# Performance work log

Measured on AMD Instinct MI355X. Metric: run time of the kernel, lower is better.

The kernel has to match this reference:

```python
import jax, jax.numpy as jnp
import numpy as np

N_HEAD, D_MODEL, D_HEAD = 16, 1024, 64
SCALE = 1.0 / (D_HEAD ** 0.5)
LN_EPS = 1e-5


def _rel_shift(x):
    # x: [b, n, i, j] -> Transformer-XL relative shift
    b, n, i, j = x.shape
    zero_pad = jnp.zeros((b, n, i, 1), x.dtype)
    x_padded = jnp.concatenate([zero_pad, x], axis=3).reshape(b, n, j + 1, i)
    return x_padded[:, :, 1:, :].reshape(b, n, i, j)


def setup_inputs() -> dict:
    key = jax.random.key(0)
    ks = jax.random.split(key, 16)
    qlen, bsz, mem_len = 1024, 2, 1024
    klen = qlen + mem_len
    rlen = klen
    s = 0.02
    inp = {
        'w': jax.random.normal(ks[0], (qlen, bsz, D_MODEL), jnp.float32),
        'r': jax.random.normal(ks[1], (rlen, D_MODEL), jnp.float32),
        'mems': jax.random.normal(ks[2], (mem_len, bsz, D_MODEL), jnp.float32),
        'r_w_bias': s * jax.random.normal(ks[3], (N_HEAD, D_HEAD), jnp.float32),
        'r_r_bias': s * jax.random.normal(ks[4], (N_HEAD, D_HEAD), jnp.float32),
        # causal mask with memory offset: position i attends to j <= i + mem_len
        'attn_mask': jnp.triu(jnp.ones((qlen, klen), bool), k=1 + mem_len),
        'Wq': s * jax.random.normal(ks[5], (D_MODEL, N_HEAD * D_HEAD), jnp.float32),
        'bq': jnp.zeros((N_HEAD * D_HEAD,), jnp.float32),
        'Wk': s * jax.random.normal(ks[6], (D_MODEL, N_HEAD * D_HEAD), jnp.float32),
        'bk': jnp.zeros((N_HEAD * D_HEAD,), jnp.float32),
        'Wv': s * jax.random.normal(ks[7], (D_MODEL, N_HEAD * D_HEAD), jnp.float32),
        'bv': jnp.zeros((N_HEAD * D_HEAD,), jnp.float32),
        'Wr': s * jax.random.normal(ks[8], (D_MODEL, N_HEAD * D_HEAD), jnp.float32),
        'br': jnp.zeros((N_HEAD * D_HEAD,), jnp.float32),
        'Wo': s * jax.random.normal(ks[9], (N_HEAD * D_HEAD, D_MODEL), jnp.float32),
        'bo': jnp.zeros((D_MODEL,), jnp.float32),
        'ln_g': jnp.ones((D_MODEL,), jnp.float32),
        'ln_b': jnp.zeros((D_MODEL,), jnp.float32),
    }
    return inp


def reference(w, r, mems, r_w_bias, r_r_bias, Wq, bq, Wk, bk, Wv, bv, Wr, br, Wo, bo, ln_g, ln_b, attn_mask):
    qlen, bsz, _ = w.shape
    cat = jnp.concatenate([mems, w], axis=0)                      # [klen, b, d_model]
    klen = cat.shape[0]
    q = (cat @ Wq + bq)[-qlen:].reshape(qlen, bsz, N_HEAD, D_HEAD)
    k = (cat @ Wk + bk).reshape(klen, bsz, N_HEAD, D_HEAD)
    v = (cat @ Wv + bv).reshape(klen, bsz, N_HEAD, D_HEAD)
    rk = (r @ Wr + br).reshape(-1, N_HEAD, D_HEAD)               # [rlen, n, d]

    AC = jnp.einsum('ibnd,jbnd->bnij', q + r_w_bias, k)          # content term
    BD = _rel_shift(jnp.einsum('ibnd,jnd->bnij', q + r_r_bias, rk))  # relative term
    attn_score = SCALE * (AC + BD)                                # [b, n, i, j]
    attn_score = jnp.where(attn_mask[None, None, :, :], -jnp.inf, attn_score)
    attn_prob = jax.nn.softmax(attn_score, axis=3)
    attn_vec = jnp.einsum('bnij,jbnd->ibnd', attn_prob, v).reshape(qlen, bsz, N_HEAD * D_HEAD)
    attn_out = attn_vec @ Wo + bo

    res = w + attn_out                                            # post-LN (pre_lnorm=False)
    mu = jnp.mean(res, axis=-1, keepdims=True)
    var = jnp.var(res, axis=-1, keepdims=True)
    return (res - mu) / jnp.sqrt(var + LN_EPS) * ln_g + ln_b
```

## Files before the change

### kernel.cpp

```cpp
#include <hip/hip_runtime.h>
#include <math.h>

#define N_HEADC 16
#define D_MODELC 1024
#define D_HEADC 64
#define QLENC 1024
#define BSZC 2
#define MEMLENC 1024
#define KLENC 2048
#define SCALEC 0.125f
#define SL2C 0.18033688011112042f
#define LN_EPSC 1e-5f
#define RINGC 192

typedef __attribute__((ext_vector_type(8))) short short8;
typedef __attribute__((ext_vector_type(4))) float f32x4;

#define MFMA16(a, b, c) __builtin_amdgcn_mfma_f32_16x16x32_bf16((a), (b), (c), 0, 0, 0)

__device__ inline unsigned short f2bf(float x) {
    union { float f; unsigned int u; } c; c.f = x;
    unsigned int r = c.u + 0x7FFFu + ((c.u >> 16) & 1u);
    return (unsigned short)(r >> 16);
}
__device__ inline float bf2f(short s) {
    union { unsigned int u; float f; } c; c.u = ((unsigned int)(unsigned short)s) << 16;
    return c.f;
}

__device__ __forceinline__ void load_lds16(const short* g, short* l) {
    __builtin_amdgcn_global_load_lds(
        (const __attribute__((address_space(1))) void*)g,
        (__attribute__((address_space(3))) void*)l,
        16, 0, 0);
}

__global__ __launch_bounds__(256) void cast_cat_kernel(
    const float* __restrict__ s0, const float* __restrict__ s1, int splitElems,
    short* __restrict__ dst)
{
    int idx = (blockIdx.x * 256 + threadIdx.x) * 8;
    const float* src = (idx < splitElems) ? (s0 + idx) : (s1 + (idx - splitElems));
    short8 o;
    #pragma unroll
    for (int e = 0; e < 8; ++e) o[e] = (short)f2bf(src[e]);
    *(short8*)(dst + idx) = o;
}

__global__ __launch_bounds__(256) void tcast5_kernel(
    const float* __restrict__ W0, const float* __restrict__ W1,
    const float* __restrict__ W2, const float* __restrict__ W3,
    const float* __restrict__ W4,
    short* __restrict__ D0, short* __restrict__ D1, short* __restrict__ D2,
    short* __restrict__ D3, short* __restrict__ D4)
{
    __shared__ short tile[64][72];
    const float* W; short* D;
    switch (blockIdx.z) {
        case 0: W = W0; D = D0; break;
        case 1: W = W1; D = D1; break;
        case 2: W = W2; D = D2; break;
        case 3: W = W3; D = D3; break;
        default: W = W4; D = D4; break;
    }
    const int t = threadIdx.x;
    const int n0 = blockIdx.x * 64, k0 = blockIdx.y * 64;
    #pragma unroll
    for (int it = 0; it < 2; ++it) {
        int idx = t + it * 256;
        int kl = idx >> 3, c8 = idx & 7;
        const float* src = W + (size_t)(k0 + kl) * D_MODELC + n0 + c8 * 8;
        short8 s;
        #pragma unroll
        for (int e = 0; e < 8; ++e) s[e] = (short)f2bf(src[e]);
        *(short8*)&tile[kl][c8 * 8] = s;
    }
    __syncthreads();
    #pragma unroll
    for (int it = 0; it < 2; ++it) {
        int idx = t + it * 256;
        int nl = idx >> 3, c8 = idx & 7;
        short8 s;
        #pragma unroll
        for (int e = 0; e < 8; ++e) s[e] = tile[c8 * 8 + e][nl];
        *(short8*)(D + (size_t)(n0 + nl) * D_MODELC + k0 + c8 * 8) = s;
    }
}

__global__ __launch_bounds__(256) void vtrans_kernel(
    const short* __restrict__ v_bf, short* __restrict__ vt)
{
    __shared__ short tile[64][72];
    const int t = threadIdx.x;
    const int j0 = blockIdx.x * 64;
    const int bn = blockIdx.y;
    const int b = bn & 1, n = bn >> 1;
    #pragma unroll
    for (int it = 0; it < 2; ++it) {
        int idx = t + it * 256;
        int jl = idx >> 3, c8 = idx & 7;
        short8 s = *(const short8*)(v_bf + ((size_t)(j0 + jl) * 2 + b) * D_MODELC + n * 64 + c8 * 8);
        *(short8*)&tile[jl][c8 * 8] = s;
    }
    __syncthreads();
    #pragma unroll
    for (int it = 0; it < 2; ++it) {
        int idx = t + it * 256;
        int dl = idx >> 3, c8 = idx & 7;
        short8 s;
        #pragma unroll
        for (int e = 0; e < 8; ++e) s[e] = tile[c8 * 8 + e][dl];
        *(short8*)(vt + ((size_t)(b * 16 + n) * 64 + dl) * (size_t)KLENC + j0 + c8 * 8) = s;
    }
}

__global__ __launch_bounds__(256, 3) void proj_gemm_kernel(
    const short* __restrict__ cat, const short* __restrict__ rin,
    const short* __restrict__ WqT, const short* __restrict__ WkT,
    const short* __restrict__ WvT, const short* __restrict__ WrT,
    const float* __restrict__ bq, const float* __restrict__ bk,
    const float* __restrict__ bv, const float* __restrict__ br,
    const float* __restrict__ rwb, const float* __restrict__ rrb,
    short* __restrict__ qw, short* __restrict__ qr,
    short* __restrict__ kb, short* __restrict__ vb, short* __restrict__ rk)
{
    __shared__ short As[128][32];
    __shared__ short Bs[128][32];

    const int lin = blockIdx.y * 8 + blockIdx.x;
    const int sw  = (lin & 7) * 96 + (lin >> 3);
    const int bx  = sw & 7;
    const int by  = sw >> 3;

    const short* A; const short* Bt; const float* bias; int yt, mode;
    if (by < 32)      { A = cat;                         Bt = WkT; bias = bk; yt = by;      mode = 0; }
    else if (by < 64) { A = cat;                         Bt = WvT; bias = bv; yt = by - 32; mode = 1; }
    else if (by < 80) { A = cat + (size_t)2048 * 1024;   Bt = WqT; bias = bq; yt = by - 64; mode = 2; }
    else              { A = rin;                         Bt = WrT; bias = br; yt = by - 80; mode = 3; }

    const int row0 = yt * 128, col0 = bx * 128;
    const int t = threadIdx.x;
    const int lane = t & 63, wid = t >> 6;
    const int row16 = lane & 15, g8 = lane >> 4;
    const int wr = wid >> 1, wc = wid & 1;

    f32x4 acc[4][4];
    #pragma unroll
    for (int m = 0; m < 4; ++m)
        #pragma unroll
        for (int nn = 0; nn < 4; ++nn)
            acc[m][nn] = (f32x4){0.f, 0.f, 0.f, 0.f};

    short* AsB = &As[0][0] + wid * 1024;
    short* BsB = &Bs[0][0] + wid * 1024;
    const int srow4 = lane >> 2;
    const int cs4 = (lane & 3) ^ ((lane >> 3) & 3);
    const short* Ag = A  + (size_t)(row0 + wid * 32 + srow4) * D_MODELC + cs4 * 8;
    const short* Bg = Bt + (size_t)(col0 + wid * 32 + srow4) * D_MODELC + cs4 * 8;
    const int xc2 = (row16 >> 1) & 3;

    for (int k0 = 0; k0 < D_MODELC; k0 += 32) {
        load_lds16(Ag + k0,              AsB);
        load_lds16(Ag + k0 + 16 * 1024,  AsB + 512);
        load_lds16(Bg + k0,              BsB);
        load_lds16(Bg + k0 + 16 * 1024,  BsB + 512);
        __syncthreads();
        short8 af[4], bfr[4];
        #pragma unroll
        for (int m = 0; m < 4; ++m)
            af[m] = *(const short8*)&As[wr * 64 + m * 16 + row16][(g8 ^ xc2) * 8];
        #pragma unroll
        for (int nn = 0; nn < 4; ++nn)
            bfr[nn] = *(const short8*)&Bs[wc * 64 + nn * 16 + row16][(g8 ^ xc2) * 8];
        #pragma unroll
        for (int m = 0; m < 4; ++m)
            #pragma unroll
            for (int nn = 0; nn < 4; ++nn)
                acc[m][nn] = MFMA16(af[m], bfr[nn], acc[m][nn]);
        __syncthreads();
    }

    float bvv[4], w1[4], w2[4];
    #pragma unroll
    for (int nn = 0; nn < 4; ++nn) {
        int c = col0 + wc * 64 + nn * 16 + row16;
        bvv[nn] = bias[c];
        w1[nn] = rwb[c];
        w2[nn] = rrb[c];
    }
    if (mode == 2) {
        #pragma unroll
        for (int m = 0; m < 4; ++m)
            #pragma unroll
            for (int nn = 0; nn < 4; ++nn) {
                int c = col0 + wc * 64 + nn * 16 + row16;
                #pragma unroll
                for (int reg = 0; reg < 4; ++reg) {
                    int r = row0 + wr * 64 + m * 16 + g8 * 4 + reg;
                    float v = acc[m][nn][reg] + bvv[nn];
                    qw[(size_t)r * D_MODELC + c] = (short)f2bf(v + w1[nn]);
                    qr[(size_t)r * D_MODELC + c] = (short)f2bf(v + w2[nn]);
                }
            }
    } else {
        short* C = (mode == 0) ? kb : (mode == 1) ? vb : rk;
        #pragma unroll
        for (int m = 0; m < 4; ++m)
            #pragma unroll
            for (int nn = 0; nn < 4; ++nn) {
                int c = col0 + wc * 64 + nn * 16 + row16;
                #pragma unroll
                for (int reg = 0; reg < 4; ++reg) {
                    int r = row0 + wr * 64 + m * 16 + g8 * 4 + reg;
                    C[(size_t)r * D_MODELC + c] = (short)f2bf(acc[m][nn][reg] + bvv[nn]);
                }
            }
    }
}

__global__ __launch_bounds__(256, 3) void wo_gemm_kernel(
    const short* __restrict__ A, const short* __restrict__ Bt,
    float* __restrict__ out0, float* __restrict__ out1)
{
    __shared__ short As[128][32];
    __shared__ short Bs[128][32];
    const int kz = blockIdx.z;
    float* C = kz ? out1 : out0;
    const int row0 = blockIdx.y * 128, col0 = blockIdx.x * 128;
    const int t = threadIdx.x;
    const int lane = t & 63, wid = t >> 6;
    const int row16 = lane & 15, g8 = lane >> 4;
    const int wr = wid >> 1, wc = wid & 1;

    f32x4 acc[4][4];
    #pragma unroll
    for (int m = 0; m < 4; ++m)
        #pragma unroll
        for (int nn = 0; nn < 4; ++nn)
            acc[m][nn] = (f32x4){0.f, 0.f, 0.f, 0.f};

    short* AsB = &As[0][0] + wid * 1024;
    short* BsB = &Bs[0][0] + wid * 1024;
    const int srow4 = lane >> 2;
    const int cs4 = (lane & 3) ^ ((lane >> 3) & 3);
    const short* Ag = A  + (size_t)(row0 + wid * 32 + srow4) * D_MODELC + cs4 * 8;
    const short* Bg = Bt + (size_t)(col0 + wid * 32 + srow4) * D_MODELC + cs4 * 8;
    const int xc2 = (row16 >> 1) & 3;

    const int kbase = kz * 512;
    for (int k0 = kbase; k0 < kbase + 512; k0 += 32) {
        load_lds16(Ag + k0,             AsB);
        load_lds16(Ag + k0 + 16 * 1024, AsB + 512);
        load_lds16(Bg + k0,             BsB);
        load_lds16(Bg + k0 + 16 * 1024, BsB + 512);
        __syncthreads();
        short8 af[4], bfr[4];
        #pragma unroll
        for (int m = 0; m < 4; ++m)
            af[m] = *(const short8*)&As[wr * 64 + m * 16 + row16][(g8 ^ xc2) * 8];
        #pragma unroll
        for (int nn = 0; nn < 4; ++nn)
            bfr[nn] = *(const short8*)&Bs[wc * 64 + nn * 16 + row16][(g8 ^ xc2) * 8];
        #pragma unroll
        for (int m = 0; m < 4; ++m)
            #pragma unroll
            for (int nn = 0; nn < 4; ++nn)
                acc[m][nn] = MFMA16(af[m], bfr[nn], acc[m][nn]);
        __syncthreads();
    }

    #pragma unroll
    for (int m = 0; m < 4; ++m)
        #pragma unroll
        for (int nn = 0; nn < 4; ++nn) {
            int c = col0 + wc * 64 + nn * 16 + row16;
            #pragma unroll
            for (int reg = 0; reg < 4; ++reg) {
                int r = row0 + wr * 64 + m * 16 + g8 * 4 + reg;
                C[(size_t)r * D_MODELC + c] = acc[m][nn][reg];
            }
        }
}

__global__ __launch_bounds__(256, 2) void attn_mfma_kernel(
    const short* __restrict__ qw, const short* __restrict__ qr,
    const short* __restrict__ kb, const short* __restrict__ rkb,
    const short* __restrict__ vt, short* __restrict__ av)
{
    __shared__ short Kl[2][64][64];
    __shared__ short Vl[64][64];
    __shared__ short Rl[RINGC][64];
    __shared__ short pun[4][1600];
    __shared__ float scb[4][16];

    const int wave = threadIdx.x >> 6, lane = threadIdx.x & 63;
    const int row16 = lane & 15, g8 = lane >> 4;
    const int srow = lane >> 3, chk = lane & 7;
    const int swz = srow & 7;

    const int lin = blockIdx.y * 16 + blockIdx.x;
    const int xcd = lin & 7;
    const int u   = lin >> 3;
    const int v   = u & 31;
    const int bn  = xcd * 4 + (v >> 3);
    const int tt  = v & 7;
    const int ic  = (u >> 5) ? (15 - tt) : tt;
    const int b = bn & 1, n = bn >> 1;
    const int i0 = ic * 64;
    const int i0w = i0 + wave * 16;

    short8 qwf[2], qrf[2];
    #pragma unroll
    for (int ks = 0; ks < 2; ++ks) {
        size_t off = ((size_t)(i0w + row16) * 2 + b) * D_MODELC + n * 64 + ks * 32 + g8 * 8;
        qwf[ks] = *(const short8*)(qw + off);
        qrf[ks] = *(const short8*)(qr + off);
    }

    #pragma unroll
    for (int t = 0; t < 2; ++t) {
        int rr = wave * 16 + t * 8;
        int j  = rr + srow;
        int cs = chk ^ swz;
        load_lds16(kb + ((size_t)j * 2 + b) * D_MODELC + n * 64 + cs * 8, &Kl[0][rr][0]);
    }
    {
        const int p0 = 960 - i0;
        #pragma unroll
        for (int t = 0; t < 4; ++t) {
            int jrb_ = p0 + wave * 32 + t * 8;
            int slotb = jrb_ % RINGC;
            int jr = jrb_ + srow;
            int jc = jr < KLENC ? jr : KLENC - 1;
            int cs = chk ^ swz;
            load_lds16(rkb + (size_t)jc * D_MODELC + n * 64 + cs * 8, &Rl[slotb][0]);
        }
    }

    f32x4 accO[4];
    #pragma unroll
    for (int dt = 0; dt < 4; ++dt) accO[dt] = (f32x4){0.f, 0.f, 0.f, 0.f};
    float m = -INFINITY, lsum = 0.f;

    const int T = (i0 + 63 + MEMLENC + 64) >> 6;
    const int r7 = row16 & 7;

    __syncthreads();

    for (int s = 0; s < T; ++s) {
        const int j0 = s * 64;
        const int cur = s & 1, nxt = cur ^ 1;

        #pragma unroll
        for (int t = 0; t < 2; ++t) {
            int rr = wave * 16 + t * 8;
            int j  = j0 + 64 + rr + srow;
            if (j > KLENC - 1) j = KLENC - 1;
            int cs = chk ^ swz;
            load_lds16(kb + ((size_t)j * 2 + b) * D_MODELC + n * 64 + cs * 8, &Kl[nxt][rr][0]);
        }
        {
            const int nb = j0 + 1088 - i0;
            #pragma unroll
            for (int t = 0; t < 2; ++t) {
                int jrb_ = nb + wave * 16 + t * 8;
                int slotb = jrb_ % RINGC;
                int jr = jrb_ + srow;
                int jc = jr < KLENC ? jr : KLENC - 1;
                int cs = chk ^ swz;
                load_lds16(rkb + (size_t)jc * D_MODELC + n * 64 + cs * 8, &Rl[slotb][0]);
            }
        }
        #pragma unroll
        for (int t = 0; t < 2; ++t) {
            int rr = wave * 16 + t * 8;
            int cs = chk ^ swz;
            load_lds16(vt + ((size_t)((b * 16 + n) * 64 + rr + srow)) * KLENC + j0 + cs * 8,
                       &Vl[rr][0]);
        }

        f32x4 st[4];
        #pragma unroll
        for (int jt = 0; jt < 4; ++jt) {
            st[jt] = (f32x4){0.f, 0.f, 0.f, 0.f};
            const short* kr = &Kl[cur][jt * 16 + row16][0];
            st[jt] = MFMA16(*(const short8*)(kr + ((g8 ^ r7) * 8)),       qwf[0], st[jt]);
            st[jt] = MFMA16(*(const short8*)(kr + (((4 + g8) ^ r7) * 8)), qwf[1], st[jt]);
        }

        const int jrb_w = j0 - i0w + 1008;
        const int sb = jrb_w % RINGC;
        short* bdT = &pun[wave][0];
        #pragma unroll
        for (int rt = 0; rt < 5; ++rt) {
            int rsl = sb + rt * 16 + row16;
            if (rsl >= RINGC) rsl -= RINGC;
            const short* rr = &Rl[rsl][0];
            f32x4 bd = (f32x4){0.f, 0.f, 0.f, 0.f};
            bd = MFMA16(*(const short8*)(rr + ((g8 ^ r7) * 8)),       qrf[0], bd);
            bd = MFMA16(*(const short8*)(rr + (((4 + g8) ^ r7) * 8)), qrf[1], bd);
            #pragma unroll
            for (int e = 0; e < 4; ++e)
                bdT[(rt * 16 + g8 * 4 + e) * 20 + row16] = (short)f2bf(bd[e]);
        }

        float sl[4][4];
        #pragma unroll
        for (int jt = 0; jt < 4; ++jt)
            #pragma unroll
            for (int reg = 0; reg < 4; ++reg) {
                const int jl = jt * 16 + g8 * 4 + reg;
                float vv = st[jt][reg] + bf2f(bdT[(jl + 15 - row16) * 20 + row16]);
                sl[jt][reg] = (j0 + jl > i0w + row16 + MEMLENC) ? -INFINITY : vv * SL2C;
            }

        float mx0 = fmaxf(fmaxf(sl[0][0], sl[0][1]), fmaxf(sl[0][2], sl[0][3]));
        float mx1 = fmaxf(fmaxf(sl[1][0], sl[1][1]), fmaxf(sl[1][2], sl[1][3]));
        float mx2 = fmaxf(fmaxf(sl[2][0], sl[2][1]), fmaxf(sl[2][2], sl[2][3]));
        float mx3 = fmaxf(fmaxf(sl[3][0], sl[3][1]), fmaxf(sl[3][2], sl[3][3]));
        float mx = fmaxf(fmaxf(mx0, mx1), fmaxf(mx2, mx3));
        mx = fmaxf(mx, __shfl_xor(mx, 16, 64));
        mx = fmaxf(mx, __shfl_xor(mx, 32, 64));

        if (__any(mx > m + 8.f)) {
            float mn = fmaxf(m, mx);
            float sc = exp2f(m - mn);
            m = mn;
            lsum *= sc;
            if (lane < 16) scb[wave][lane] = sc;
            float4 s4 = *(const float4*)&scb[wave][g8 * 4];
            #pragma unroll
            for (int dt = 0; dt < 4; ++dt) {
                accO[dt][0] *= s4.x; accO[dt][1] *= s4.y;
                accO[dt][2] *= s4.z; accO[dt][3] *= s4.w;
            }
        }

        float ps = 0.f;
        #pragma unroll
        for (int jt = 0; jt < 4; ++jt)
            #pragma unroll
            for (int reg = 0; reg < 4; ++reg) {
                float p = exp2f(sl[jt][reg] - m);
                sl[jt][reg] = p;
                ps += p;
            }
        ps += __shfl_xor(ps, 16, 64);
        ps += __shfl_xor(ps, 32, 64);
        lsum += ps;
        short* pP = &pun[wave][0];
        #pragma unroll
        for (int jt = 0; jt < 4; ++jt)
            #pragma unroll
            for (int reg = 0; reg < 4; ++reg) {
                const int ch = (jt * 2 + (g8 >> 1)) ^ r7;
                pP[row16 * 64 + ch * 8 + (g8 & 1) * 4 + reg] = (short)f2bf(sl[jt][reg]);
            }

        __syncthreads();

        #pragma unroll
        for (int ks2 = 0; ks2 < 2; ++ks2) {
            short8 pf = *(const short8*)&pP[row16 * 64 + (((ks2 * 4 + g8) ^ r7) * 8)];
            #pragma unroll
            for (int dt = 0; dt < 4; ++dt) {
                const short* vp = &Vl[dt * 16 + row16][(((ks2 * 4 + g8) ^ r7) * 8)];
                accO[dt] = MFMA16(pf, *(const short8*)vp, accO[dt]);
            }
        }

        __syncthreads();
    }

    if (lane < 16) scb[wave][lane] = lsum;
    float4 l4 = *(const float4*)&scb[wave][g8 * 4];
    float rl4[4] = {1.f / l4.x, 1.f / l4.y, 1.f / l4.z, 1.f / l4.w};
    #pragma unroll
    for (int dt = 0; dt < 4; ++dt)
        #pragma unroll
        for (int reg = 0; reg < 4; ++reg) {
            size_t o = ((size_t)(i0w + g8 * 4 + reg) * 2 + b) * D_MODELC + n * 64 + dt * 16 + row16;
            av[o] = (short)f2bf(accO[dt][reg] * rl4[reg]);
        }
}

__global__ __launch_bounds__(256) void ln_kernel(
    const float* __restrict__ w, const float* __restrict__ ao0,
    const float* __restrict__ ao1, const float* __restrict__ bo,
    const float* __restrict__ g, const float* __restrict__ bb,
    float* __restrict__ out)
{
    __shared__ float red[2][4];
    const int row = blockIdx.x;
    const int lane = threadIdx.x & 63;
    const int wv = threadIdx.x >> 6;
    const size_t base = (size_t)row * D_MODELC;
    const int c = threadIdx.x * 4;

    float4 xw = *(const float4*)&w[base + c];
    float4 x0 = *(const float4*)&ao0[base + c];
    float4 x1 = *(const float4*)&ao1[base + c];
    float4 xb = *(const float4*)&bo[c];
    float x[4] = {xw.x + x0.x + x1.x + xb.x, xw.y + x0.y + x1.y + xb.y,
                  xw.z + x0.z + x1.z + xb.z, xw.w + x0.w + x1.w + xb.w};

    float sum = x[0] + x[1] + x[2] + x[3];
    float ssq = x[0]*x[0] + x[1]*x[1] + x[2]*x[2] + x[3]*x[3];
    #pragma unroll
    for (int off = 32; off > 0; off >>= 1) {
        sum += __shfl_xor(sum, off, 64);
        ssq += __shfl_xor(ssq, off, 64);
    }
    if (lane == 0) { red[0][wv] = sum; red[1][wv] = ssq; }
    __syncthreads();
    sum = red[0][0] + red[0][1] + red[0][2] + red[0][3];
    ssq = red[1][0] + red[1][1] + red[1][2] + red[1][3];

    const float mu = sum * (1.0f / D_MODELC);
    const float var = ssq * (1.0f / D_MODELC) - mu * mu;
    const float rstd = rsqrtf(var + LN_EPSC);

    float4 o;
    o.x = (x[0] - mu) * rstd * g[c] + bb[c];
    o.y = (x[1] - mu) * rstd * g[c+1] + bb[c+1];
    o.z = (x[2] - mu) * rstd * g[c+2] + bb[c+2];
    o.w = (x[3] - mu) * rstd * g[c+3] + bb[c+3];
    *(float4*)&out[base + c] = o;
}

extern "C" void kernel_launch(void* const* d_in, const int* in_sizes, int n_in,
                              void* d_out, int out_size, void* d_ws, size_t ws_size,
                              hipStream_t stream)
{
    const float* w    = (const float*)d_in[0];
    const float* r    = (const float*)d_in[1];
    const float* mems = (const float*)d_in[2];
    const float* rwb  = (const float*)d_in[3];
    const float* rrb  = (const float*)d_in[4];
    const float* Wq = (const float*)d_in[6];
    const float* bq = (const float*)d_in[7];
    const float* Wk = (const float*)d_in[8];
    const float* bk = (const float*)d_in[9];
    const float* Wv = (const float*)d_in[10];
    const float* bv = (const float*)d_in[11];
    const float* Wr = (const float*)d_in[12];
    const float* br = (const float*)d_in[13];
    const float* Wo = (const float*)d_in[14];
    const float* bo = (const float*)d_in[15];
    const float* ln_g = (const float*)d_in[16];
    const float* ln_b = (const float*)d_in[17];
    float* out = (float*)d_out;

    char* ws = (char*)d_ws;
    const size_t MB = 1ull << 20;
    short* cat_bf = (short*)(ws + 0 * MB);
    short* r_bf   = (short*)(ws + 8 * MB);
    short* Wq_t   = (short*)(ws + 12 * MB);
    short* Wk_t   = (short*)(ws + 14 * MB);
    short* Wv_t   = (short*)(ws + 16 * MB);
    short* Wr_t   = (short*)(ws + 18 * MB);
    short* Wo_t   = (short*)(ws + 20 * MB);
    short* qw_bf  = (short*)(ws + 22 * MB);
    short* qr_bf  = (short*)(ws + 26 * MB);
    short* k_bf   = (short*)(ws + 30 * MB);
    short* v_bf   = (short*)(ws + 38 * MB);
    short* rk_bf  = (short*)(ws + 46 * MB);
    short* vt     = (short*)(ws + 50 * MB);
    short* av_bf  = (short*)(ws + 58 * MB);
    float* ao0    = (float*)v_bf;
    float* ao1    = (float*)k_bf;

    dim3 blk(256);

    cast_cat_kernel<<<dim3(2048), blk, 0, stream>>>(mems, w, 2048 * 1024, cat_bf);
    cast_cat_kernel<<<dim3(1024), blk, 0, stream>>>(r, r, 1 << 30, r_bf);

    tcast5_kernel<<<dim3(16, 16, 5), blk, 0, stream>>>(
        Wq, Wk, Wv, Wr, Wo, Wq_t, Wk_t, Wv_t, Wr_t, Wo_t);

    proj_gemm_kernel<<<dim3(8, 96), blk, 0, stream>>>(
        cat_bf, r_bf, Wq_t, Wk_t, Wv_t, Wr_t,
        bq, bk, bv, br, rwb, rrb,
        qw_bf, qr_bf, k_bf, v_bf, rk_bf);

    vtrans_kernel<<<dim3(32, 32), blk, 0, stream>>>(v_bf, vt);

    attn_mfma_kernel<<<dim3(16, 32), blk, 0, stream>>>(
        qw_bf, qr_bf, k_bf, rk_bf, vt, av_bf);

    wo_gemm_kernel<<<dim3(8, 16, 2), blk, 0, stream>>>(av_bf, Wo_t, ao0, ao1);

    ln_kernel<<<dim3(2048), blk, 0, stream>>>(w, ao0, ao1, bo, ln_g, ln_b, out);
}
```

Before: 159.8 us.

## Split attention key range across two blocks and merge partial softmax results

Result: slower. 178.3 us (+11.6%).

```diff
diff --git a/kernel.cpp b/kernel.cpp
--- a/kernel.cpp
+++ b/kernel.cpp
@@ -11,7 +11,6 @@
 #define SCALEC 0.125f
 #define SL2C 0.18033688011112042f
 #define LN_EPSC 1e-5f
-#define RINGC 192
 
 typedef __attribute__((ext_vector_type(8))) short short8;
 typedef __attribute__((ext_vector_type(4))) float f32x4;
@@ -22,6 +21,14 @@
     union { float f; unsigned int u; } c; c.f = x;
     unsigned int r = c.u + 0x7FFFu + ((c.u >> 16) & 1u);
     return (unsigned short)(r >> 16);
+}
+__device__ inline unsigned short f2bft(float x) {
+    union { float f; unsigned int u; } c; c.f = x;
+    return (unsigned short)(c.u >> 16);
+}
+__device__ inline unsigned int pk2(float a, float b) {
+    union { float f; unsigned int u; } x, y; x.f = a; y.f = b;
+    return (x.u >> 16) | (y.u & 0xFFFF0000u);
 }
 __device__ inline float bf2f(short s) {
     union { unsigned int u; float f; } c; c.u = ((unsigned int)(unsigned short)s) << 16;
@@ -282,29 +289,30 @@
         }
 }
 
-__global__ __launch_bounds__(256, 2) void attn_mfma_kernel(
+__global__ __launch_bounds__(256, 4) void attn_mfma_kernel(
     const short* __restrict__ qw, const short* __restrict__ qr,
     const short* __restrict__ kb, const short* __restrict__ rkb,
-    const short* __restrict__ vt, short* __restrict__ av)
+    const short* __restrict__ vt,
+    float* __restrict__ Op0, float* __restrict__ Op1, float* __restrict__ ml)
 {
     __shared__ short Kl[2][64][64];
     __shared__ short Vl[64][64];
-    __shared__ short Rl[RINGC][64];
-    __shared__ short pun[4][1600];
+    __shared__ short pun[4][1680];
     __shared__ float scb[4][16];
 
     const int wave = threadIdx.x >> 6, lane = threadIdx.x & 63;
     const int row16 = lane & 15, g8 = lane >> 4;
     const int srow = lane >> 3, chk = lane & 7;
-    const int swz = srow & 7;
 
     const int lin = blockIdx.y * 16 + blockIdx.x;
     const int xcd = lin & 7;
     const int u   = lin >> 3;
-    const int v   = u & 31;
+    const int jh  = u & 1;
+    const int w2  = u >> 1;
+    const int v   = w2 & 31;
     const int bn  = xcd * 4 + (v >> 3);
     const int tt  = v & 7;
-    const int ic  = (u >> 5) ? (15 - tt) : tt;
+    const int ic  = (w2 >> 5) ? (15 - tt) : tt;
     const int b = bn & 1, n = bn >> 1;
     const int i0 = ic * 64;
     const int i0w = i0 + wave * 16;
@@ -320,21 +328,9 @@
     #pragma unroll
     for (int t = 0; t < 2; ++t) {
         int rr = wave * 16 + t * 8;
-        int j  = rr + srow;
-        int cs = chk ^ swz;
+        int j  = jh * 64 + rr + srow;
+        int cs = chk ^ srow;
         load_lds16(kb + ((size_t)j * 2 + b) * D_MODELC + n * 64 + cs * 8, &Kl[0][rr][0]);
-    }
-    {
-        const int p0 = 960 - i0;
-        #pragma unroll
-        for (int t = 0; t < 4; ++t) {
-            int jrb_ = p0 + wave * 32 + t * 8;
-            int slotb = jrb_ % RINGC;
-            int jr = jrb_ + srow;
-            int jc = jr < KLENC ? jr : KLENC - 1;
-            int cs = chk ^ swz;
-            load_lds16(rkb + (size_t)jc * D_MODELC + n * 64 + cs * 8, &Rl[slotb][0]);
-        }
     }
 
     f32x4 accO[4];
@@ -347,34 +343,34 @@
 
     __syncthreads();
 
-    for (int s = 0; s < T; ++s) {
+    int cur = 0;
+    for (int s = jh; s < T; s += 2) {
         const int j0 = s * 64;
-        const int cur = s & 1, nxt = cur ^ 1;
+        const int nxt = cur ^ 1;
+
+        const int jrb_w = j0 - i0w + 1008;
+        short8 rkf0[5], rkf1[5];
+        #pragma unroll
+        for (int rt = 0; rt < 5; ++rt) {
+            int jr = jrb_w + rt * 16 + row16;
+            if (jr > KLENC - 1) jr = KLENC - 1;
+            const short* rp = rkb + (size_t)jr * D_MODELC + n * 64 + g8 * 8;
+            rkf0[rt] = *(const short8*)rp;
+            rkf1[rt] = *(const short8*)(rp + 32);
+        }
 
         #pragma unroll
         for (int t = 0; t < 2; ++t) {
             int rr = wave * 16 + t * 8;
-            int j  = j0 + 64 + rr + srow;
+            int j  = j0 + 128 + rr + srow;
             if (j > KLENC - 1) j = KLENC - 1;
-            int cs = chk ^ swz;
+            int cs = chk ^ srow;
             load_lds16(kb + ((size_t)j * 2 + b) * D_MODELC + n * 64 + cs * 8, &Kl[nxt][rr][0]);
-        }
-        {
-            const int nb = j0 + 1088 - i0;
-            #pragma unroll
-            for (int t = 0; t < 2; ++t) {
-                int jrb_ = nb + wave * 16 + t * 8;
-                int slotb = jrb_ % RINGC;
-                int jr = jrb_ + srow;
-                int jc = jr < KLENC ? jr : KLENC - 1;
-                int cs = chk ^ swz;
-                load_lds16(rkb + (size_t)jc * D_MODELC + n * 64 + cs * 8, &Rl[slotb][0]);
-            }
         }
         #pragma unroll
         for (int t = 0; t < 2; ++t) {
             int rr = wave * 16 + t * 8;
-            int cs = chk ^ swz;
+            int cs = chk ^ srow;
             load_lds16(vt + ((size_t)((b * 16 + n) * 64 + rr + srow)) * KLENC + j0 + cs * 8,
                        &Vl[rr][0]);
         }
@@ -388,20 +384,15 @@
             st[jt] = MFMA16(*(const short8*)(kr + (((4 + g8) ^ r7) * 8)), qwf[1], st[jt]);
         }
 
-        const int jrb_w = j0 - i0w + 1008;
-        const int sb = jrb_w % RINGC;
         short* bdT = &pun[wave][0];
         #pragma unroll
         for (int rt = 0; rt < 5; ++rt) {
-            int rsl = sb + rt * 16 + row16;
-            if (rsl >= RINGC) rsl -= RINGC;
-            const short* rr = &Rl[rsl][0];
             f32x4 bd = (f32x4){0.f, 0.f, 0.f, 0.f};
-            bd = MFMA16(*(const short8*)(rr + ((g8 ^ r7) * 8)),       qrf[0], bd);
-            bd = MFMA16(*(const short8*)(rr + (((4 + g8) ^ r7) * 8)), qrf[1], bd);
+            bd = MFMA16(rkf0[rt], qrf[0], bd);
+            bd = MFMA16(rkf1[rt], qrf[1], bd);
             #pragma unroll
             for (int e = 0; e < 4; ++e)
-                bdT[(rt * 16 + g8 * 4 + e) * 20 + row16] = (short)f2bf(bd[e]);
+                bdT[(rt * 16 + g8 * 4 + e) * 21 + row16] = (short)f2bft(bd[e]);
         }
 
         float sl[4][4];
@@ -410,7 +401,7 @@
             #pragma unroll
             for (int reg = 0; reg < 4; ++reg) {
                 const int jl = jt * 16 + g8 * 4 + reg;
-                float vv = st[jt][reg] + bf2f(bdT[(jl + 15 - row16) * 20 + row16]);
+                float vv = st[jt][reg] + bf2f(bdT[(jl + 15 - row16) * 21 + row16]);
                 sl[jt][reg] = (j0 + jl > i0w + row16 + MEMLENC) ? -INFINITY : vv * SL2C;
             }
 
@@ -445,17 +436,18 @@
                 sl[jt][reg] = p;
                 ps += p;
             }
+        short* pP = &pun[wave][0];
+        #pragma unroll
+        for (int jt = 0; jt < 4; ++jt) {
+            const int ch = (jt * 2 + (g8 >> 1)) ^ r7;
+            uint2 pkd;
+            pkd.x = pk2(sl[jt][0], sl[jt][1]);
+            pkd.y = pk2(sl[jt][2], sl[jt][3]);
+            *(uint2*)&pP[row16 * 64 + ch * 8 + (g8 & 1) * 4] = pkd;
+        }
         ps += __shfl_xor(ps, 16, 64);
         ps += __shfl_xor(ps, 32, 64);
         lsum += ps;
-        short* pP = &pun[wave][0];
-        #pragma unroll
-        for (int jt = 0; jt < 4; ++jt)
-            #pragma unroll
-            for (int reg = 0; reg < 4; ++reg) {
-                const int ch = (jt * 2 + (g8 >> 1)) ^ r7;
-                pP[row16 * 64 + ch * 8 + (g8 & 1) * 4 + reg] = (short)f2bf(sl[jt][reg]);
-            }
 
         __syncthreads();
 
@@ -470,18 +462,38 @@
         }
 
         __syncthreads();
-    }
-
-    if (lane < 16) scb[wave][lane] = lsum;
-    float4 l4 = *(const float4*)&scb[wave][g8 * 4];
-    float rl4[4] = {1.f / l4.x, 1.f / l4.y, 1.f / l4.z, 1.f / l4.w};
+        cur = nxt;
+    }
+
+    if (g8 == 0) {
+        int g = ((i0w + row16) * 2 + b) * 16 + n;
+        ml[jh * 65536 + g]         = m;
+        ml[jh * 65536 + 32768 + g] = lsum;
+    }
+    float* Op = jh ? Op1 : Op0;
     #pragma unroll
     for (int dt = 0; dt < 4; ++dt)
         #pragma unroll
         for (int reg = 0; reg < 4; ++reg) {
-            size_t o = ((size_t)(i0w + g8 * 4 + reg) * 2 + b) * D_MODELC + n * 64 + dt * 16 + row16;
-            av[o] = (short)f2bf(accO[dt][reg] * rl4[reg]);
-        }
+            int g = ((i0w + g8 * 4 + reg) * 2 + b) * 16 + n;
+            Op[(size_t)g * 64 + dt * 16 + row16] = accO[dt][reg];
+        }
+}
+
+__global__ __launch_bounds__(256) void attn_merge_kernel(
+    const float* __restrict__ Op0, const float* __restrict__ Op1,
+    const float* __restrict__ ml, short* __restrict__ av)
+{
+    const int g = blockIdx.x * 4 + (threadIdx.x >> 6);
+    const int d = threadIdx.x & 63;
+    float m0 = ml[g],         l0 = ml[32768 + g];
+    float m1 = ml[65536 + g], l1 = ml[98304 + g];
+    float M  = fmaxf(m0, m1);
+    float e0 = exp2f(m0 - M), e1 = exp2f(m1 - M);
+    float rden = 1.f / (l0 * e0 + l1 * e1);
+    size_t o = (size_t)g * 64 + d;
+    float val = (Op0[o] * e0 + Op1[o] * e1) * rden;
+    av[o] = (short)f2bf(val);
 }
 
 __global__ __launch_bounds__(256) void ln_kernel(
@@ -567,6 +579,9 @@
     short* rk_bf  = (short*)(ws + 46 * MB);
     short* vt     = (short*)(ws + 50 * MB);
     short* av_bf  = (short*)(ws + 58 * MB);
+    float* Op0    = (float*)cat_bf;
+    float* mlp    = (float*)r_bf;
+    float* Op1    = (float*)Wq_t;
     float* ao0    = (float*)v_bf;
     float* ao1    = (float*)k_bf;
 
@@ -585,8 +600,10 @@
 
     vtrans_kernel<<<dim3(32, 32), blk, 0, stream>>>(v_bf, vt);
 
-    attn_mfma_kernel<<<dim3(16, 32), blk, 0, stream>>>(
-        qw_bf, qr_bf, k_bf, rk_bf, vt, av_bf);
+    attn_mfma_kernel<<<dim3(16, 64), blk, 0, stream>>>(
+        qw_bf, qr_bf, k_bf, rk_bf, vt, Op0, Op1, mlp);
+
+    attn_merge_kernel<<<dim3(8192), blk, 0, stream>>>(Op0, Op1, mlp, av_bf);
 
     wo_gemm_kernel<<<dim3(8, 16, 2), blk, 0, stream>>>(av_bf, Wo_t, ao0, ao1);
 
```

## Double-buffer V tiles, drop mid-loop barrier, pack bf16 LDS stores

Applied to the files above, without the earlier changes.

Result: faster. 156.5 us (-2.0%).

```diff
diff --git a/kernel.cpp b/kernel.cpp
--- a/kernel.cpp
+++ b/kernel.cpp
@@ -23,6 +23,10 @@
     unsigned int r = c.u + 0x7FFFu + ((c.u >> 16) & 1u);
     return (unsigned short)(r >> 16);
 }
+__device__ inline unsigned int pk2(float a, float b) {
+    union { float f; unsigned int u; } x, y; x.f = a; y.f = b;
+    return (x.u >> 16) | (y.u & 0xFFFF0000u);
+}
 __device__ inline float bf2f(short s) {
     union { unsigned int u; float f; } c; c.u = ((unsigned int)(unsigned short)s) << 16;
     return c.f;
@@ -288,9 +292,9 @@
     const short* __restrict__ vt, short* __restrict__ av)
 {
     __shared__ short Kl[2][64][64];
-    __shared__ short Vl[64][64];
+    __shared__ short Vl[2][64][64];
     __shared__ short Rl[RINGC][64];
-    __shared__ short pun[4][1600];
+    __shared__ short pun[4][1376];
     __shared__ float scb[4][16];
 
     const int wave = threadIdx.x >> 6, lane = threadIdx.x & 63;
@@ -323,6 +327,8 @@
         int j  = rr + srow;
         int cs = chk ^ swz;
         load_lds16(kb + ((size_t)j * 2 + b) * D_MODELC + n * 64 + cs * 8, &Kl[0][rr][0]);
+        load_lds16(vt + ((size_t)((b * 16 + n) * 64 + rr + srow)) * KLENC + cs * 8,
+                   &Vl[0][rr][0]);
     }
     {
         const int p0 = 960 - i0;
@@ -347,9 +353,10 @@
 
     __syncthreads();
 
+    int cur = 0;
     for (int s = 0; s < T; ++s) {
         const int j0 = s * 64;
-        const int cur = s & 1, nxt = cur ^ 1;
+        const int nxt = cur ^ 1;
 
         #pragma unroll
         for (int t = 0; t < 2; ++t) {
@@ -371,14 +378,18 @@
                 load_lds16(rkb + (size_t)jc * D_MODELC + n * 64 + cs * 8, &Rl[slotb][0]);
             }
         }
-        #pragma unroll
-        for (int t = 0; t < 2; ++t) {
-            int rr = wave * 16 + t * 8;
-            int cs = chk ^ swz;
-            load_lds16(vt + ((size_t)((b * 16 + n) * 64 + rr + srow)) * KLENC + j0 + cs * 8,
-                       &Vl[rr][0]);
-        }
-
+        {
+            const int jsrc = (j0 + 64 <= KLENC - 64) ? (j0 + 64) : (KLENC - 64);
+            #pragma unroll
+            for (int t = 0; t < 2; ++t) {
+                int rr = wave * 16 + t * 8;
+                int cs = chk ^ swz;
+                load_lds16(vt + ((size_t)((b * 16 + n) * 64 + rr + srow)) * KLENC + jsrc + cs * 8,
+                           &Vl[nxt][rr][0]);
+            }
+        }
+
+        __builtin_amdgcn_s_setprio(1);
         f32x4 st[4];
         #pragma unroll
         for (int jt = 0; jt < 4; ++jt) {
@@ -399,10 +410,12 @@
             f32x4 bd = (f32x4){0.f, 0.f, 0.f, 0.f};
             bd = MFMA16(*(const short8*)(rr + ((g8 ^ r7) * 8)),       qrf[0], bd);
             bd = MFMA16(*(const short8*)(rr + (((4 + g8) ^ r7) * 8)), qrf[1], bd);
-            #pragma unroll
-            for (int e = 0; e < 4; ++e)
-                bdT[(rt * 16 + g8 * 4 + e) * 20 + row16] = (short)f2bf(bd[e]);
-        }
+            uint2 wv;
+            wv.x = pk2(bd[0], bd[1]);
+            wv.y = pk2(bd[2], bd[3]);
+            *(uint2*)&bdT[row16 * 84 + rt * 16 + g8 * 4] = wv;
+        }
+        __builtin_amdgcn_s_setprio(0);
 
         float sl[4][4];
         #pragma unroll
@@ -410,7 +423,7 @@
             #pragma unroll
             for (int reg = 0; reg < 4; ++reg) {
                 const int jl = jt * 16 + g8 * 4 + reg;
-                float vv = st[jt][reg] + bf2f(bdT[(jl + 15 - row16) * 20 + row16]);
+                float vv = st[jt][reg] + bf2f(bdT[row16 * 84 + jl + 15 - row16]);
                 sl[jt][reg] = (j0 + jl > i0w + row16 + MEMLENC) ? -INFINITY : vv * SL2C;
             }
 
@@ -445,31 +458,33 @@
                 sl[jt][reg] = p;
                 ps += p;
             }
+        short* pP = &pun[wave][0];
+        #pragma unroll
+        for (int jt = 0; jt < 4; ++jt) {
+            const int ch = (jt * 2 + (g8 >> 1)) ^ r7;
+            uint2 pkd;
+            pkd.x = pk2(sl[jt][0], sl[jt][1]);
+            pkd.y = pk2(sl[jt][2], sl[jt][3]);
+            *(uint2*)&pP[row16 * 64 + ch * 8 + (g8 & 1) * 4] = pkd;
+        }
         ps += __shfl_xor(ps, 16, 64);
         ps += __shfl_xor(ps, 32, 64);
         lsum += ps;
-        short* pP = &pun[wave][0];
-        #pragma unroll
-        for (int jt = 0; jt < 4; ++jt)
-            #pragma unroll
-            for (int reg = 0; reg < 4; ++reg) {
-                const int ch = (jt * 2 + (g8 >> 1)) ^ r7;
-                pP[row16 * 64 + ch * 8 + (g8 & 1) * 4 + reg] = (short)f2bf(sl[jt][reg]);
-            }
-
-        __syncthreads();
-
+
+        __builtin_amdgcn_s_setprio(1);
         #pragma unroll
         for (int ks2 = 0; ks2 < 2; ++ks2) {
             short8 pf = *(const short8*)&pP[row16 * 64 + (((ks2 * 4 + g8) ^ r7) * 8)];
             #pragma unroll
             for (int dt = 0; dt < 4; ++dt) {
-                const short* vp = &Vl[dt * 16 + row16][(((ks2 * 4 + g8) ^ r7) * 8)];
+                const short* vp = &Vl[cur][dt * 16 + row16][(((ks2 * 4 + g8) ^ r7) * 8)];
                 accO[dt] = MFMA16(pf, *(const short8*)vp, accO[dt]);
             }
         }
+        __builtin_amdgcn_s_setprio(0);
 
         __syncthreads();
+        cur = nxt;
     }
 
     if (lane < 16) scb[wave][lane] = lsum;
```
